# Kernel optimization log

Measured on AMD Instinct MI355X. Metric: run time of the kernel, lower is better.

The kernel has to match this reference:

```python
import jax, jax.numpy as jnp
import numpy as np

EPS_NORM = 1e-12  # F.normalize eps
SINK_EPS = 0.1    # entropic regularization
THRESH = 0.01
MAX_ITERS = 100


def _l2_normalize(x):
    n = jnp.linalg.norm(x, axis=1, keepdims=True)
    return x / jnp.maximum(n, EPS_NORM)


def _sinkhorn(K, u, v):
    # K: [M, N], u: [M], v: [N]. Mirrors the torch loop with early stop on err < thresh.
    def cond(state):
        i, r, c, err = state
        return jnp.logical_and(i < MAX_ITERS, err >= THRESH)

    def body(state):
        i, r, c, _ = state
        r0 = r
        r = u / (K @ c)          # [M]
        c = v / (K.T @ r)        # [N]
        err = jnp.mean(jnp.abs(r - r0))
        return (i + 1, r, c, err)

    init = (jnp.int32(0), jnp.ones_like(u), jnp.ones_like(v), jnp.float32(1e9))
    _, r, c, _ = jax.lax.while_loop(cond, body, init)
    return jnp.outer(r, c) * K   # [M, N]


def _ot(src, tgt):
    # src: [M, D] (gt cluster centers), tgt: [N, D] (local features)
    s = _l2_normalize(src)
    t = _l2_normalize(tgt)
    sim = s @ t.T                         # [M, N], differentiable
    M, N = sim.shape
    u = jnp.full((M,), 1.0 / M, sim.dtype)
    v = jnp.full((N,), 1.0 / N, sim.dtype)
    K = jax.lax.stop_gradient(jnp.exp(-(1.0 - sim) / SINK_EPS))  # no_grad in torch
    T = jax.lax.stop_gradient(_sinkhorn(K, u, v))
    return jnp.sum(T * sim)


def setup_inputs() -> dict:
    key = jax.random.key(0)
    k1, k2, k3, k4 = jax.random.split(key, 4)
    E, B, D = 3, 4096, 1024
    M, N = 5, 256
    return {
        "feature": jax.random.normal(k1, (E, B, D), jnp.float32),
        "gt": jax.random.normal(k2, (E, B, D), jnp.float32),
        "gt_local": jax.random.normal(k3, (E, M, D), jnp.float32),
        "feature_local": jax.random.normal(k4, (E, N, D), jnp.float32),
    }


def reference(feature, gt, gt_local, feature_local):
    E = feature.shape[0]
    # global term: (1/E) * sum_e mean_b sum_d feature*gt
    loss_global = jnp.mean(jnp.sum(feature * gt, axis=-1))
    # local OT term per extractor: OT(gt_local, feature_local) * 2, then / E
    ot_vals = jax.vmap(_ot)(gt_local, feature_local)  # [E]
    loss_local = jnp.sum(ot_vals * 2.0) / E
    return loss_global + loss_local * 0.1
```

## Files before the change

### kernel.cpp

```cpp
#include <hip/hip_runtime.h>
#include <math.h>

typedef float f32x4 __attribute__((ext_vector_type(4)));

#define NSIM_BLOCKS 48
#define NDOT_BLOCKS 2048
#define THREADS 256
#define TOTAL_F4 3145728
#define DOT_STRIDE (NDOT_BLOCKS * THREADS)

__global__ __launch_bounds__(256) void fused_main(
    const f32x4* __restrict__ f4, const f32x4* __restrict__ g4,
    const float* __restrict__ gt_local, const float* __restrict__ feat_local,
    float* __restrict__ ws_partials, float* __restrict__ ws_sim)
{
    __shared__ float s_sh[5120];
    const int tid = threadIdx.x;
    const int lane = tid & 63;
    const int wid = tid >> 6;

    if (blockIdx.x >= NSIM_BLOCKS) {
        const int base = (blockIdx.x - NSIM_BLOCKS) * THREADS + tid;
        f32x4 a0 = __builtin_nontemporal_load(&f4[base + 0 * DOT_STRIDE]);
        f32x4 b0 = __builtin_nontemporal_load(&g4[base + 0 * DOT_STRIDE]);
        f32x4 a1 = __builtin_nontemporal_load(&f4[base + 1 * DOT_STRIDE]);
        f32x4 b1 = __builtin_nontemporal_load(&g4[base + 1 * DOT_STRIDE]);
        f32x4 a2 = __builtin_nontemporal_load(&f4[base + 2 * DOT_STRIDE]);
        f32x4 b2 = __builtin_nontemporal_load(&g4[base + 2 * DOT_STRIDE]);
        f32x4 a3 = __builtin_nontemporal_load(&f4[base + 3 * DOT_STRIDE]);
        f32x4 b3 = __builtin_nontemporal_load(&g4[base + 3 * DOT_STRIDE]);
        f32x4 a4 = __builtin_nontemporal_load(&f4[base + 4 * DOT_STRIDE]);
        f32x4 b4 = __builtin_nontemporal_load(&g4[base + 4 * DOT_STRIDE]);
        f32x4 a5 = __builtin_nontemporal_load(&f4[base + 5 * DOT_STRIDE]);
        f32x4 b5 = __builtin_nontemporal_load(&g4[base + 5 * DOT_STRIDE]);
        f32x4 p0 = a0 * b0 + a1 * b1;
        f32x4 p1 = a2 * b2 + a3 * b3;
        f32x4 p2 = a4 * b4 + a5 * b5;
        f32x4 p = p0 + p1 + p2;
        float acc = p.x + p.y + p.z + p.w;
        #pragma unroll
        for (int o = 32; o; o >>= 1) acc += __shfl_xor(acc, o);
        if (lane == 0) s_sh[wid] = acc;
        __syncthreads();
        if (tid == 0)
            ws_partials[blockIdx.x - NSIM_BLOCKS] =
                s_sh[0] + s_sh[1] + s_sh[2] + s_sh[3];
    } else {
        const int e = blockIdx.x >> 4;
        const int chunk = blockIdx.x & 15;
        const f32x4* sbase = (const f32x4*)(gt_local + e * 5120);
        #pragma unroll
        for (int k = 0; k < 5; ++k)
            ((f32x4*)s_sh)[tid + 256 * k] = sbase[tid + 256 * k];
        __syncthreads();
        for (int m = wid; m < 5; m += 4) {
            float acc = 0.f;
            #pragma unroll
            for (int k = 0; k < 16; ++k) {
                float v = s_sh[m * 1024 + lane + 64 * k];
                acc += v * v;
            }
            #pragma unroll
            for (int o = 32; o; o >>= 1) acc += __shfl_xor(acc, o);
            const float rinv = 1.f / fmaxf(sqrtf(acc), 1e-12f);
            #pragma unroll
            for (int k = 0; k < 16; ++k)
                s_sh[m * 1024 + lane + 64 * k] *= rinv;
        }
        __syncthreads();
        for (int rr = 0; rr < 4; ++rr) {
            const int n = chunk * 16 + wid * 4 + rr;
            const float* trow = feat_local + (e * 256 + n) * 1024;
            float a0 = 0.f, a1 = 0.f, a2 = 0.f, a3 = 0.f, a4 = 0.f, at = 0.f;
            #pragma unroll
            for (int k = 0; k < 16; ++k) {
                const int d = lane + 64 * k;
                const float tv = trow[d];
                at += tv * tv;
                a0 += tv * s_sh[d];
                a1 += tv * s_sh[1024 + d];
                a2 += tv * s_sh[2048 + d];
                a3 += tv * s_sh[3072 + d];
                a4 += tv * s_sh[4096 + d];
            }
            #pragma unroll
            for (int o = 32; o; o >>= 1) {
                at += __shfl_xor(at, o);
                a0 += __shfl_xor(a0, o);
                a1 += __shfl_xor(a1, o);
                a2 += __shfl_xor(a2, o);
                a3 += __shfl_xor(a3, o);
                a4 += __shfl_xor(a4, o);
            }
            if (lane == 0) {
                const float rnt = 1.f / fmaxf(sqrtf(at), 1e-12f);
                float* dst = ws_sim + e * 5 * 256 + n;
                dst[0]    = a0 * rnt;
                dst[256]  = a1 * rnt;
                dst[512]  = a2 * rnt;
                dst[768]  = a3 * rnt;
                dst[1024] = a4 * rnt;
            }
        }
    }
}

__global__ __launch_bounds__(256) void finalize_kernel(
    const float* __restrict__ ws_partials, const float* __restrict__ ws_sim,
    float* __restrict__ out)
{
    __shared__ float ot_sh[3];
    __shared__ double g_sh;
    const int tid = threadIdx.x;
    const int lane = tid & 63;
    const int wid = tid >> 6;

    if (wid < 3) {
        const int e = wid;
        float K[5][4], S[5][4];
        #pragma unroll
        for (int m = 0; m < 5; ++m)
            #pragma unroll
            for (int j = 0; j < 4; ++j) {
                const float s = ws_sim[(e * 5 + m) * 256 + lane + 64 * j];
                S[m][j] = s;
                K[m][j] = expf(-(1.0f - s) / 0.1f);
            }
        float r[5] = {1.f, 1.f, 1.f, 1.f, 1.f};
        float c[4] = {1.f, 1.f, 1.f, 1.f};
        float err;
        int it = 0;
        do {
            float r0[5];
            #pragma unroll
            for (int m = 0; m < 5; ++m) r0[m] = r[m];
            #pragma unroll
            for (int m = 0; m < 5; ++m) {
                float p = K[m][0] * c[0] + K[m][1] * c[1] +
                          K[m][2] * c[2] + K[m][3] * c[3];
                #pragma unroll
                for (int o = 32; o; o >>= 1) p += __shfl_xor(p, o);
                r[m] = 0.2f / p;
            }
            #pragma unroll
            for (int j = 0; j < 4; ++j) {
                const float q = K[0][j] * r[0] + K[1][j] * r[1] +
                                K[2][j] * r[2] + K[3][j] * r[3] +
                                K[4][j] * r[4];
                c[j] = (1.0f / 256.0f) / q;
            }
            err = (fabsf(r[0] - r0[0]) + fabsf(r[1] - r0[1]) +
                   fabsf(r[2] - r0[2]) + fabsf(r[3] - r0[3]) +
                   fabsf(r[4] - r0[4])) * 0.2f;
            ++it;
        } while (it < 100 && err >= 0.01f);

        float ot = 0.f;
        #pragma unroll
        for (int m = 0; m < 5; ++m)
            #pragma unroll
            for (int j = 0; j < 4; ++j)
                ot += r[m] * c[j] * K[m][j] * S[m][j];
        #pragma unroll
        for (int o = 32; o; o >>= 1) ot += __shfl_xor(ot, o);
        if (lane == 0) ot_sh[e] = ot;
    } else {
        double acc = 0.0;
        #pragma unroll
        for (int k = 0; k < 32; ++k) acc += (double)ws_partials[lane + 64 * k];
        #pragma unroll
        for (int o = 32; o; o >>= 1) acc += __shfl_xor(acc, o);
        if (lane == 0) g_sh = acc;
    }
    __syncthreads();
    if (tid == 0) {
        const float loss_global = (float)(g_sh / 12288.0);
        const float loss_local = (ot_sh[0] + ot_sh[1] + ot_sh[2]) * 2.0f / 3.0f;
        out[0] = loss_global + 0.1f * loss_local;
    }
}

extern "C" void kernel_launch(void* const* d_in, const int* in_sizes, int n_in,
                              void* d_out, int out_size, void* d_ws, size_t ws_size,
                              hipStream_t stream) {
    const f32x4* f4 = (const f32x4*)d_in[0];
    const f32x4* g4 = (const f32x4*)d_in[1];
    const float* gt_local = (const float*)d_in[2];
    const float* feat_local = (const float*)d_in[3];
    float* ws_partials = (float*)d_ws;
    float* ws_sim = ws_partials + NDOT_BLOCKS;
    float* out = (float*)d_out;

    hipLaunchKernelGGL(fused_main, dim3(NSIM_BLOCKS + NDOT_BLOCKS), dim3(THREADS),
                       0, stream, f4, g4, gt_local, feat_local, ws_partials, ws_sim);
    hipLaunchKernelGGL(finalize_kernel, dim3(1), dim3(THREADS), 0, stream,
                       ws_partials, ws_sim, out);
}
```

Baseline: 131.6 us.

## Fuse finalize into main kernel via last-block atomic counter

Merges the single-block finalize kernel into the main kernel: each block increments a global atomic counter, and the last block to finish runs the Sinkhorn solve and the global reduction. A memset resets the counter before each launch. The dot-product grid also shrinks to 2000 blocks with a guarded seventh load, and the loads switch from nontemporal to ordinary cached loads. This removes one kernel launch and its dependency gap, but adds a memset node, fences and atomic serialization at the tail.

```diff
diff --git a/kernel.cpp b/kernel.cpp
--- a/kernel.cpp
+++ b/kernel.cpp
@@ -4,47 +4,56 @@
 typedef float f32x4 __attribute__((ext_vector_type(4)));
 
 #define NSIM_BLOCKS 48
-#define NDOT_BLOCKS 2048
+#define NDOT_BLOCKS 2000
+#define NBLOCKS (NSIM_BLOCKS + NDOT_BLOCKS)
 #define THREADS 256
 #define TOTAL_F4 3145728
 #define DOT_STRIDE (NDOT_BLOCKS * THREADS)
 
-__global__ __launch_bounds__(256) void fused_main(
+#define WS_SIM_OFF 2048
+#define WS_CTR_OFF 6144
+
+__global__ __launch_bounds__(256) void fused_all(
     const f32x4* __restrict__ f4, const f32x4* __restrict__ g4,
     const float* __restrict__ gt_local, const float* __restrict__ feat_local,
-    float* __restrict__ ws_partials, float* __restrict__ ws_sim)
+    float* __restrict__ ws, float* __restrict__ out)
 {
     __shared__ float s_sh[5120];
+    float* red_sh = s_sh;
+    int* flag_sh = (int*)&s_sh[8];
+    float* ot_sh = &s_sh[12];
+    double* g_sh = (double*)&s_sh[16];
+
+    float* ws_partials = ws;
+    float* ws_sim = ws + WS_SIM_OFF;
+    unsigned int* counter = (unsigned int*)(ws + WS_CTR_OFF);
+
     const int tid = threadIdx.x;
     const int lane = tid & 63;
     const int wid = tid >> 6;
 
     if (blockIdx.x >= NSIM_BLOCKS) {
         const int base = (blockIdx.x - NSIM_BLOCKS) * THREADS + tid;
-        f32x4 a0 = __builtin_nontemporal_load(&f4[base + 0 * DOT_STRIDE]);
-        f32x4 b0 = __builtin_nontemporal_load(&g4[base + 0 * DOT_STRIDE]);
-        f32x4 a1 = __builtin_nontemporal_load(&f4[base + 1 * DOT_STRIDE]);
-        f32x4 b1 = __builtin_nontemporal_load(&g4[base + 1 * DOT_STRIDE]);
-        f32x4 a2 = __builtin_nontemporal_load(&f4[base + 2 * DOT_STRIDE]);
-        f32x4 b2 = __builtin_nontemporal_load(&g4[base + 2 * DOT_STRIDE]);
-        f32x4 a3 = __builtin_nontemporal_load(&f4[base + 3 * DOT_STRIDE]);
-        f32x4 b3 = __builtin_nontemporal_load(&g4[base + 3 * DOT_STRIDE]);
-        f32x4 a4 = __builtin_nontemporal_load(&f4[base + 4 * DOT_STRIDE]);
-        f32x4 b4 = __builtin_nontemporal_load(&g4[base + 4 * DOT_STRIDE]);
-        f32x4 a5 = __builtin_nontemporal_load(&f4[base + 5 * DOT_STRIDE]);
-        f32x4 b5 = __builtin_nontemporal_load(&g4[base + 5 * DOT_STRIDE]);
-        f32x4 p0 = a0 * b0 + a1 * b1;
-        f32x4 p1 = a2 * b2 + a3 * b3;
-        f32x4 p2 = a4 * b4 + a5 * b5;
-        f32x4 p = p0 + p1 + p2;
+        f32x4 p = {0.f, 0.f, 0.f, 0.f};
+        #pragma unroll
+        for (int k = 0; k < 6; ++k) {
+            const f32x4 a = f4[base + k * DOT_STRIDE];
+            const f32x4 b = g4[base + k * DOT_STRIDE];
+            p += a * b;
+        }
+        if (base + 6 * DOT_STRIDE < TOTAL_F4) {
+            const f32x4 a = f4[base + 6 * DOT_STRIDE];
+            const f32x4 b = g4[base + 6 * DOT_STRIDE];
+            p += a * b;
+        }
         float acc = p.x + p.y + p.z + p.w;
         #pragma unroll
         for (int o = 32; o; o >>= 1) acc += __shfl_xor(acc, o);
-        if (lane == 0) s_sh[wid] = acc;
+        if (lane == 0) red_sh[wid] = acc;
         __syncthreads();
         if (tid == 0)
             ws_partials[blockIdx.x - NSIM_BLOCKS] =
-                s_sh[0] + s_sh[1] + s_sh[2] + s_sh[3];
+                red_sh[0] + red_sh[1] + red_sh[2] + red_sh[3];
     } else {
         const int e = blockIdx.x >> 4;
         const int chunk = blockIdx.x & 15;
@@ -102,18 +111,18 @@
                 dst[1024] = a4 * rnt;
             }
         }
-    }
-}
-
-__global__ __launch_bounds__(256) void finalize_kernel(
-    const float* __restrict__ ws_partials, const float* __restrict__ ws_sim,
-    float* __restrict__ out)
-{
-    __shared__ float ot_sh[3];
-    __shared__ double g_sh;
-    const int tid = threadIdx.x;
-    const int lane = tid & 63;
-    const int wid = tid >> 6;
+        __syncthreads();
+    }
+
+    if (tid == 0) {
+        __threadfence();
+        flag_sh[0] = (atomicAdd(counter, 1u) == NBLOCKS - 1);
+    }
+    __syncthreads();
+    if (!flag_sh[0]) return;
+
+    __threadfence();
+    __syncthreads();
 
     if (wid < 3) {
         const int e = wid;
@@ -164,17 +173,20 @@
         #pragma unroll
         for (int o = 32; o; o >>= 1) ot += __shfl_xor(ot, o);
         if (lane == 0) ot_sh[e] = ot;
-    } else {
+    } else if (wid == 3) {
         double acc = 0.0;
         #pragma unroll
-        for (int k = 0; k < 32; ++k) acc += (double)ws_partials[lane + 64 * k];
+        for (int k = 0; k < 32; ++k) {
+            const int idx = lane + 64 * k;
+            if (idx < NDOT_BLOCKS) acc += (double)ws_partials[idx];
+        }
         #pragma unroll
         for (int o = 32; o; o >>= 1) acc += __shfl_xor(acc, o);
-        if (lane == 0) g_sh = acc;
+        if (lane == 0) g_sh[0] = acc;
     }
     __syncthreads();
     if (tid == 0) {
-        const float loss_global = (float)(g_sh / 12288.0);
+        const float loss_global = (float)(g_sh[0] / 12288.0);
         const float loss_local = (ot_sh[0] + ot_sh[1] + ot_sh[2]) * 2.0f / 3.0f;
         out[0] = loss_global + 0.1f * loss_local;
     }
@@ -187,12 +199,11 @@
     const f32x4* g4 = (const f32x4*)d_in[1];
     const float* gt_local = (const float*)d_in[2];
     const float* feat_local = (const float*)d_in[3];
-    float* ws_partials = (float*)d_ws;
-    float* ws_sim = ws_partials + NDOT_BLOCKS;
+    float* ws = (float*)d_ws;
     float* out = (float*)d_out;
 
-    hipLaunchKernelGGL(fused_main, dim3(NSIM_BLOCKS + NDOT_BLOCKS), dim3(THREADS),
-                       0, stream, f4, g4, gt_local, feat_local, ws_partials, ws_sim);
-    hipLaunchKernelGGL(finalize_kernel, dim3(1), dim3(THREADS), 0, stream,
-                       ws_partials, ws_sim, out);
+    hipMemsetAsync((char*)d_ws + WS_CTR_OFF * sizeof(float), 0,
+                   sizeof(unsigned int), stream);
+    hipLaunchKernelGGL(fused_all, dim3(NBLOCKS), dim3(THREADS), 0, stream,
+                       f4, g4, gt_local, feat_local, ws, out);
 }
```

New measurement: 219.6 us. +66.9%, slower.
